# Kernel optimization log

Measured on AMD Instinct MI355X. Metric: run time of the kernel, lower is better.

Reference implementation:

```python
import jax, jax.numpy as jnp
import numpy as np

N_NODES = 100000
N_EDGES = 1600000
IN_DIM, HID_DIM, OUT_DIM = 128, 128, 64


def setup_inputs() -> dict:
    key = jax.random.key(0)
    ks = jax.random.split(key, 5)
    x = jax.random.normal(ks[0], (N_NODES, IN_DIM), dtype=jnp.float32)
    edge_index = jax.random.randint(ks[1], (2, N_EDGES), 0, N_NODES, dtype=jnp.int64)
    W1 = jax.random.normal(ks[2], (IN_DIM, HID_DIM), dtype=jnp.float32) * (1.0 / np.sqrt(IN_DIM))
    b1 = jnp.zeros((HID_DIM,), dtype=jnp.float32)
    W2 = jax.random.normal(ks[3], (HID_DIM, OUT_DIM), dtype=jnp.float32) * (1.0 / np.sqrt(HID_DIM))
    b2 = jnp.zeros((OUT_DIM,), dtype=jnp.float32)
    return {"x": x, "edge_index": edge_index, "W1": W1, "b1": b1, "W2": W2, "b2": b2}


def _gcn_conv(h, row, col, norm, b, n_nodes):
    # h: [N, F] already linearly transformed; message = norm_e * h[src]; scatter-add to dst
    msg = h[row] * norm[:, None]                      # [E+N, F]
    out = jax.ops.segment_sum(msg, col, num_segments=n_nodes)
    return out + b


def reference(x, edge_index, W1, b1, W2, b2):
    n = x.shape[0]
    loops = jnp.arange(n, dtype=edge_index.dtype)
    row = jnp.concatenate([edge_index[0], loops])     # sources (incl. self loops)
    col = jnp.concatenate([edge_index[1], loops])     # targets
    # symmetric normalization: deg over targets with unit edge weights
    deg = jax.ops.segment_sum(jnp.ones_like(col, dtype=x.dtype), col, num_segments=n)
    dinv = jnp.where(deg > 0, jax.lax.rsqrt(jnp.maximum(deg, 1.0)), 0.0)
    norm = dinv[row] * dinv[col]                      # [E+N]
    h = jax.nn.relu(_gcn_conv(x @ W1, row, col, norm, b1, n))
    out = _gcn_conv(h @ W2, row, col, norm, b2, n)
    return out.mean(axis=0)                           # [OUT_DIM]
```

## Files before the change

kernel.cpp:

```cpp
#include <hip/hip_runtime.h>

#define N_NODES 100000
#define N_EDGES 1600000
#define IN_DIM 128
#define HID_DIM 128
#define OUT_DIM 64
#define BKT_SHIFT 7
#define BKT_SIZE 128
#define NBKT ((N_NODES + BKT_SIZE - 1) / BKT_SIZE)
#define B1 256
#define HIST_N (NBKT * B1)
#define HIST_N2 (2 * HIST_N)
#define GEMM_BLKS ((N_NODES + 127) / 128)

typedef float v2f __attribute__((ext_vector_type(2)));
typedef float v4f __attribute__((ext_vector_type(4)));
typedef short v8s __attribute__((ext_vector_type(8)));

__device__ __forceinline__ unsigned int f2bf(float f) {
  unsigned int u = __float_as_uint(f);
  return (u + 0x7FFFu + ((u >> 16) & 1u)) >> 16;
}

template <bool HI>
__device__ __forceinline__ v2f cvt8(unsigned int u) {
  return __builtin_amdgcn_cvt_pk_f32_fp8((int)u, HI);
}

__device__ __forceinline__ float wdec(unsigned int p) {
  return __uint_as_float((p >> 17) << 16);
}

__device__ __forceinline__ void load4(const void* ei, int is64, int half, int base,
                                      int* v) {
  if (is64) {
    const long long* e = (const long long*)ei + (size_t)half * N_EDGES + base;
    longlong2 a = *(const longlong2*)e;
    longlong2 b = *(const longlong2*)(e + 2);
    v[0] = (int)a.x; v[1] = (int)a.y; v[2] = (int)b.x; v[3] = (int)b.y;
  } else {
    const int* e = (const int*)ei + (size_t)half * N_EDGES + base;
    int4 a = *(const int4*)e;
    v[0] = a.x; v[1] = a.y; v[2] = a.z; v[3] = a.w;
  }
}

__device__ __forceinline__ int detect64_block(const unsigned int* ei, int* sh) {
  if (threadIdx.x == 0) *sh = 0;
  __syncthreads();
  if (ei[1 + 2 * threadIdx.x] != 0u) *sh = 1;
  __syncthreads();
  return (*sh == 0) ? 1 : 0;
}

__global__ __launch_bounds__(256) void front_kernel(const float* __restrict__ x,
                                                    const float* __restrict__ W,
                                                    const void* ei,
                                                    unsigned int* __restrict__ G,
                                                    int* hist, float* S) {
  __shared__ __align__(16) char smem[2 * 128 * 136 * 2];
  if (blockIdx.x >= GEMM_BLKS) {
    int* hd = (int*)smem;
    int* hs = hd + NBKT;
    int* sh = hs + NBKT;
    const int hb = blockIdx.x - GEMM_BLKS;
    if (hb == 0 && threadIdx.x < HID_DIM) S[threadIdx.x] = 0.f;
    const int is64 = detect64_block((const unsigned int*)ei, sh);
    for (int k = threadIdx.x; k < NBKT; k += 256) { hd[k] = 0; hs[k] = 0; }
    __syncthreads();
    for (int g = hb * 256 + threadIdx.x; g < N_EDGES / 4; g += B1 * 256) {
      int r[4], c[4];
      load4(ei, is64, 0, g * 4, r);
      load4(ei, is64, 1, g * 4, c);
#pragma unroll
      for (int k = 0; k < 4; k++) {
        atomicAdd(&hd[c[k] >> BKT_SHIFT], 1);
        atomicAdd(&hs[r[k] >> BKT_SHIFT], 1);
      }
    }
    __syncthreads();
    for (int k = threadIdx.x; k < NBKT; k += 256) {
      hist[k * B1 + hb] = hd[k];
      hist[HIST_N + k * B1 + hb] = hs[k];
    }
    return;
  }
  typedef unsigned short us_row[136];
  us_row* lx = (us_row*)smem;
  us_row* lwt = (us_row*)(smem + 128 * 136 * 2);
  const int t = threadIdx.x;
  const int row0 = blockIdx.x * 128;

  {
    const float4* W4 = (const float4*)W;
    for (int it = 0; it < 16; ++it) {
      int idx = t + 256 * it;
      int k = idx >> 5, c4 = (idx & 31) * 4;
      float4 w = W4[idx];
      lwt[c4 + 0][k] = (unsigned short)f2bf(w.x);
      lwt[c4 + 1][k] = (unsigned short)f2bf(w.y);
      lwt[c4 + 2][k] = (unsigned short)f2bf(w.z);
      lwt[c4 + 3][k] = (unsigned short)f2bf(w.w);
    }
  }
  {
    const float4* x4 = (const float4*)(x + (size_t)row0 * IN_DIM);
    for (int it = 0; it < 16; ++it) {
      int idx = t + 256 * it;
      int r = idx >> 5, kq = (idx & 31) * 4;
      float4 v = make_float4(0.f, 0.f, 0.f, 0.f);
      if (row0 + r < N_NODES) v = x4[idx];
      unsigned int p0 = (f2bf(v.y) << 16) | f2bf(v.x);
      unsigned int p1 = (f2bf(v.w) << 16) | f2bf(v.z);
      *(uint2*)&lx[r][kq] = make_uint2(p0, p1);
    }
  }
  __syncthreads();

  const int lane = t & 63;
  const int wv = t >> 6;
  const int m0 = wv * 32;
  const int lrow = lane & 15;
  const int lk = (lane >> 4) * 8;

  v4f acc[2][8];
#pragma unroll
  for (int si = 0; si < 2; si++)
#pragma unroll
    for (int n = 0; n < 8; n++) acc[si][n] = (v4f){0.f, 0.f, 0.f, 0.f};

#pragma unroll
  for (int kk = 0; kk < 128; kk += 32) {
    v8s a0 = *(const v8s*)&lx[m0 + lrow][kk + lk];
    v8s a1 = *(const v8s*)&lx[m0 + 16 + lrow][kk + lk];
#pragma unroll
    for (int n = 0; n < 8; n++) {
      v8s b = *(const v8s*)&lwt[n * 16 + lrow][kk + lk];
      acc[0][n] = __builtin_amdgcn_mfma_f32_16x16x32_bf16(a0, b, acc[0][n], 0, 0, 0);
      acc[1][n] = __builtin_amdgcn_mfma_f32_16x16x32_bf16(a1, b, acc[1][n], 0, 0, 0);
    }
  }

  unsigned char* G8 = (unsigned char*)G;
#pragma unroll
  for (int si = 0; si < 2; si++)
#pragma unroll
    for (int n = 0; n < 8; n++) {
      int colg = n * 16 + (lane & 15);
#pragma unroll
      for (int i = 0; i < 4; i++) {
        int r = row0 + m0 + si * 16 + (lane >> 4) * 4 + i;
        if (r < N_NODES) {
          float v = acc[si][n][i];
          int pk = __builtin_amdgcn_cvt_pk_fp8_f32(v, v, 0, false);
          G8[(size_t)r * HID_DIM + colg] = (unsigned char)(pk & 0xFF);
        }
      }
    }
}

__global__ void scan1_kernel(int* arr, int* bsum, int n) {
  __shared__ int tmp[256];
  int i = blockIdx.x * 256 + threadIdx.x;
  int v = (i < n) ? arr[i] : 0;
  tmp[threadIdx.x] = v;
  __syncthreads();
  for (int off = 1; off < 256; off <<= 1) {
    int t2 = (threadIdx.x >= off) ? tmp[threadIdx.x - off] : 0;
    __syncthreads();
    tmp[threadIdx.x] += t2;
    __syncthreads();
  }
  if (i < n) arr[i] = tmp[threadIdx.x] - v;
  if (threadIdx.x == 255) bsum[blockIdx.x] = tmp[255];
}

__global__ void scan2_kernel(int* bsum, int nb) {
  __shared__ int tmp[1024];
  const int t = threadIdx.x;
  int v0 = (2 * t < nb) ? bsum[2 * t] : 0;
  int v1 = (2 * t + 1 < nb) ? bsum[2 * t + 1] : 0;
  int s = v0 + v1;
  tmp[t] = s;
  __syncthreads();
  for (int off = 1; off < 1024; off <<= 1) {
    int t2 = (t >= off) ? tmp[t - off] : 0;
    __syncthreads();
    tmp[t] += t2;
    __syncthreads();
  }
  int excl = tmp[t] - s;
  if (2 * t < nb) bsum[2 * t] = excl;
  if (2 * t + 1 < nb) bsum[2 * t + 1] = excl + v0;
}

__global__ __launch_bounds__(256) void scatter_kernel(const void* ei, const int* hist,
                                                      const int* bsum,
                                                      unsigned int* pairs) {
  __shared__ int cd[NBKT], cs[NBKT], sh[1];
  const int is64 = detect64_block((const unsigned int*)ei, sh);
  for (int k = threadIdx.x; k < NBKT; k += 256) {
    cd[k] = hist[k * B1 + blockIdx.x] + bsum[k];
    cs[k] = hist[HIST_N + k * B1 + blockIdx.x] + bsum[NBKT + k];
  }
  __syncthreads();
  for (int g = blockIdx.x * 256 + threadIdx.x; g < N_EDGES / 4; g += B1 * 256) {
    int r[4], c[4];
    load4(ei, is64, 0, g * 4, r);
    load4(ei, is64, 1, g * 4, c);
#pragma unroll
    for (int k = 0; k < 4; k++) {
      int pd = atomicAdd(&cd[c[k] >> BKT_SHIFT], 1);
      pairs[pd] = ((unsigned int)(c[k] & (BKT_SIZE - 1)) << 17) | (unsigned int)r[k];
      int ps = atomicAdd(&cs[r[k] >> BKT_SHIFT], 1);
      pairs[ps] = ((unsigned int)(r[k] & (BKT_SIZE - 1)) << 17) | (unsigned int)c[k];
    }
  }
}

__global__ __launch_bounds__(256) void csrA_kernel(const int* hist, const int* bsum,
                                                   const unsigned int* pairs,
                                                   int* rowptr, float* dinv) {
  __shared__ int cnt[BKT_SIZE], sc[BKT_SIZE];
  const int k = blockIdx.x;
  const int base = hist[k * B1] + bsum[k];
  const int end = (k == NBKT - 1) ? N_EDGES : hist[(k + 1) * B1] + bsum[k + 1];
  const int nseg = end - base;
  const int l = threadIdx.x;
  if (l < BKT_SIZE) cnt[l] = 0;
  __syncthreads();
  for (int i = l; i < nseg; i += 256) atomicAdd(&cnt[pairs[base + i] >> 17], 1);
  __syncthreads();
  if (l < BKT_SIZE) sc[l] = cnt[l];
  __syncthreads();
  for (int off = 1; off < BKT_SIZE; off <<= 1) {
    int v = (l < BKT_SIZE && l >= off) ? sc[l - off] : 0;
    __syncthreads();
    if (l < BKT_SIZE) sc[l] += v;
    __syncthreads();
  }
  if (l < BKT_SIZE) {
    int excl = sc[l] - cnt[l];
    int v = k * BKT_SIZE + l;
    if (v < N_NODES) {
      rowptr[v] = base + excl;
      dinv[v] = rsqrtf((float)(cnt[l] + 1));
    }
  }
  if (k == NBKT - 1 && l == 0) rowptr[N_NODES] = N_EDGES;
}

__global__ __launch_bounds__(256) void csrBout_kernel(const int* hist, const int* bsum,
                                                      const unsigned int* pairs,
                                                      const int* __restrict__ rowptr,
                                                      const float* __restrict__ dinv,
                                                      unsigned int* __restrict__ csr,
                                                      float* __restrict__ wacc) {
  if (blockIdx.x < NBKT) {
    __shared__ int cur[BKT_SIZE];
    const int k = blockIdx.x;
    const int base = hist[k * B1] + bsum[k];
    const int end = (k == NBKT - 1) ? N_EDGES : hist[(k + 1) * B1] + bsum[k + 1];
    const int nseg = end - base;
    const int l = threadIdx.x;
    if (l < BKT_SIZE) {
      int v = k * BKT_SIZE + l;
      cur[l] = (v < N_NODES) ? rowptr[v] : 0;
    }
    __syncthreads();
    for (int i = l; i < nseg; i += 256) {
      unsigned int pk = pairs[base + i];
      unsigned int src = pk & 0x1FFFFu;
      int pos = atomicAdd(&cur[pk >> 17], 1);
      unsigned int bits = f2bf(dinv[src]);
      csr[pos] = (bits << 17) | src;
    }
    return;
  }
  __shared__ float fb[BKT_SIZE];
  const int k = blockIdx.x - NBKT;
  const int base = hist[HIST_N + k * B1] + bsum[NBKT + k];
  const int end =
      (k == NBKT - 1) ? 2 * N_EDGES : hist[HIST_N + (k + 1) * B1] + bsum[NBKT + k + 1];
  if (threadIdx.x < BKT_SIZE) fb[threadIdx.x] = 0.f;
  __syncthreads();
  for (int i = base + threadIdx.x; i < end; i += 256) {
    unsigned int pk = pairs[i];
    atomicAdd(&fb[pk >> 17], dinv[pk & 0x1FFFFu]);
  }
  __syncthreads();
  int v = k * BKT_SIZE + threadIdx.x;
  if (threadIdx.x < BKT_SIZE && v < N_NODES) wacc[v] = fb[threadIdx.x];
}

__global__ __launch_bounds__(256) void aggregate_kernel(
    const unsigned int* __restrict__ G, const int* __restrict__ rowptr,
    const unsigned int* __restrict__ csr, const float* __restrict__ dinv,
    const float* __restrict__ wacc, const float* __restrict__ b1,
    float* __restrict__ S) {
  const int lane = threadIdx.x & 63;
  const int sub = lane & 31;
  const int half = lane >> 5;
  const int wid = blockIdx.x * 4 + (threadIdx.x >> 6);
  const int nwaves = gridDim.x * 4;
  const float4 b = ((const float4*)b1)[sub];
  v2f s01 = {0.f, 0.f}, s23 = {0.f, 0.f};

  for (int c = wid; c < N_NODES; c += nwaves) {
    const int start = rowptr[c];
    const int cnum = rowptr[c + 1] - start;
    const float d = dinv[c];
    v2f a01 = {0.f, 0.f}, a23 = {0.f, 0.f};
    if (half == 0) {
      unsigned int g = G[c * 32 + sub];
      a01 = cvt8<false>(g) * d;
      a23 = cvt8<true>(g) * d;
    }
    for (int j0 = 0; j0 < cnum; j0 += 64) {
      unsigned int pkl = 0;
      if (j0 + lane < cnum)
        pkl = __builtin_nontemporal_load(&csr[start + j0 + lane]);
      const int m = min(64, cnum - j0);
      int i = 0;
      for (; i + 8 <= m; i += 8) {
        unsigned int p0 = __shfl(pkl, i + half);
        unsigned int p1 = __shfl(pkl, i + 2 + half);
        unsigned int p2 = __shfl(pkl, i + 4 + half);
        unsigned int p3 = __shfl(pkl, i + 6 + half);
        unsigned int g0 = G[(p0 & 0x1FFFFu) * 32 + sub];
        unsigned int g1 = G[(p1 & 0x1FFFFu) * 32 + sub];
        unsigned int g2 = G[(p2 & 0x1FFFFu) * 32 + sub];
        unsigned int g3 = G[(p3 & 0x1FFFFu) * 32 + sub];
        float w0 = wdec(p0), w1 = wdec(p1), w2 = wdec(p2), w3 = wdec(p3);
        a01 += cvt8<false>(g0) * w0; a23 += cvt8<true>(g0) * w0;
        a01 += cvt8<false>(g1) * w1; a23 += cvt8<true>(g1) * w1;
        a01 += cvt8<false>(g2) * w2; a23 += cvt8<true>(g2) * w2;
        a01 += cvt8<false>(g3) * w3; a23 += cvt8<true>(g3) * w3;
      }
      for (; i + 2 <= m; i += 2) {
        unsigned int p = __shfl(pkl, i + half);
        unsigned int g = G[(p & 0x1FFFFu) * 32 + sub];
        float w = wdec(p);
        a01 += cvt8<false>(g) * w;
        a23 += cvt8<true>(g) * w;
      }
      if (i < m) {
        unsigned int p = __shfl(pkl, i);
        if (half == 0) {
          unsigned int g = G[(p & 0x1FFFFu) * 32 + sub];
          float w = wdec(p);
          a01 += cvt8<false>(g) * w;
          a23 += cvt8<true>(g) * w;
        }
      }
    }
    a01.x += __shfl(a01.x, sub + 32);
    a01.y += __shfl(a01.y, sub + 32);
    a23.x += __shfl(a23.x, sub + 32);
    a23.y += __shfl(a23.y, sub + 32);
    if (half == 0) {
      float wc = d * (wacc[c] + d);
      s01.x += wc * fmaxf(fmaf(d, a01.x, b.x), 0.f);
      s01.y += wc * fmaxf(fmaf(d, a01.y, b.y), 0.f);
      s23.x += wc * fmaxf(fmaf(d, a23.x, b.z), 0.f);
      s23.y += wc * fmaxf(fmaf(d, a23.y, b.w), 0.f);
    }
  }

  __shared__ float ls[HID_DIM];
  if (threadIdx.x < HID_DIM) ls[threadIdx.x] = 0.f;
  __syncthreads();
  if (half == 0) {
    atomicAdd(&ls[4 * sub + 0], s01.x);
    atomicAdd(&ls[4 * sub + 1], s01.y);
    atomicAdd(&ls[4 * sub + 2], s23.x);
    atomicAdd(&ls[4 * sub + 3], s23.y);
  }
  __syncthreads();
  if (threadIdx.x < HID_DIM) atomicAdd(&S[threadIdx.x], ls[threadIdx.x]);
}

__global__ void finish_kernel(const float* __restrict__ S, const float* __restrict__ W2,
                              const float* __restrict__ b2, float* __restrict__ out) {
  int j = threadIdx.x;
  float acc = 0.f;
  for (int k = 0; k < HID_DIM; k++) acc += S[k] * W2[k * OUT_DIM + j];
  out[j] = acc * (1.0f / N_NODES) + b2[j];
}

extern "C" void kernel_launch(void* const* d_in, const int* in_sizes, int n_in,
                              void* d_out, int out_size, void* d_ws, size_t ws_size,
                              hipStream_t stream) {
  const float* x  = (const float*)d_in[0];
  const void*  ei = d_in[1];
  const float* W1 = (const float*)d_in[2];
  const float* b1 = (const float*)d_in[3];
  const float* W2 = (const float*)d_in[4];
  const float* b2 = (const float*)d_in[5];
  float* out = (float*)d_out;

  char* p = (char*)d_ws;
  size_t off = 0;
  auto alloc = [&](size_t bytes) -> void* {
    void* r = p + off;
    off = (off + bytes + 63) & ~(size_t)63;
    return r;
  };
  int*   hist   = (int*)alloc((size_t)HIST_N2 * 4);
  int*   bsum   = (int*)alloc(2048 * 4);
  unsigned int* pairs = (unsigned int*)alloc((size_t)2 * N_EDGES * 4);
  int*   rowptr = (int*)alloc(((size_t)N_NODES + 1) * 4);
  unsigned int* csr = (unsigned int*)alloc((size_t)N_EDGES * 4);
  float* dinv   = (float*)alloc((size_t)N_NODES * 4);
  float* wacc   = (float*)alloc((size_t)N_NODES * 4);
  float* S      = (float*)alloc(HID_DIM * 4);
  unsigned int* G = (unsigned int*)alloc((size_t)N_NODES * HID_DIM);
  (void)ws_size; (void)n_in; (void)in_sizes; (void)out_size;

  const int NBH = HIST_N2 / 256;

  front_kernel<<<GEMM_BLKS + B1, 256, 0, stream>>>(x, W1, ei, G, hist, S);
  scan1_kernel<<<NBH, 256, 0, stream>>>(hist, bsum, HIST_N2);
  scan2_kernel<<<1, 1024, 0, stream>>>(bsum, NBH);
  scatter_kernel<<<B1, 256, 0, stream>>>(ei, hist, bsum, pairs);
  csrA_kernel<<<NBKT, 256, 0, stream>>>(hist, bsum, pairs, rowptr, dinv);
  csrBout_kernel<<<2 * NBKT, 256, 0, stream>>>(hist, bsum, pairs, rowptr, dinv, csr,
                                               wacc);
  aggregate_kernel<<<2048, 256, 0, stream>>>(G, rowptr, csr, dinv, wacc, b1, S);
  finish_kernel<<<1, 64, 0, stream>>>(S, W2, b2, out);
}
```

Baseline: 291.6 us.

## Split fp8 hidden features into two column planes and aggregate each separately

The GEMM output is stored as two planes of 64 fp8 columns each, and the aggregation kernel is launched once per plane. Each wave now handles four edges at a time with 16 lanes per edge instead of two edges with 32 lanes. The aim is for each plane's gather working set (about 6.4MB) to sit better in cache, and for each gather to touch a 64-byte row segment. The cost is reading the CSR indices and metadata twice, plus a second kernel launch.

```diff
diff --git a/kernel.cpp b/kernel.cpp
--- a/kernel.cpp
+++ b/kernel.cpp
@@ -56,7 +56,7 @@
 __global__ __launch_bounds__(256) void front_kernel(const float* __restrict__ x,
                                                     const float* __restrict__ W,
                                                     const void* ei,
-                                                    unsigned int* __restrict__ G,
+                                                    unsigned char* __restrict__ G8,
                                                     int* hist, float* S) {
   __shared__ __align__(16) char smem[2 * 128 * 136 * 2];
   if (blockIdx.x >= GEMM_BLKS) {
@@ -141,19 +141,19 @@
     }
   }
 
-  unsigned char* G8 = (unsigned char*)G;
 #pragma unroll
   for (int si = 0; si < 2; si++)
 #pragma unroll
     for (int n = 0; n < 8; n++) {
       int colg = n * 16 + (lane & 15);
+      size_t pbase = (size_t)(colg >> 6) * N_NODES * 64 + (colg & 63);
 #pragma unroll
       for (int i = 0; i < 4; i++) {
         int r = row0 + m0 + si * 16 + (lane >> 4) * 4 + i;
         if (r < N_NODES) {
           float v = acc[si][n][i];
           int pk = __builtin_amdgcn_cvt_pk_fp8_f32(v, v, 0, false);
-          G8[(size_t)r * HID_DIM + colg] = (unsigned char)(pk & 0xFF);
+          G8[pbase + (size_t)r * 64] = (unsigned char)(pk & 0xFF);
         }
       }
     }
@@ -294,16 +294,16 @@
 }
 
 __global__ __launch_bounds__(256) void aggregate_kernel(
-    const unsigned int* __restrict__ G, const int* __restrict__ rowptr,
+    const unsigned int* __restrict__ Gp, const int* __restrict__ rowptr,
     const unsigned int* __restrict__ csr, const float* __restrict__ dinv,
-    const float* __restrict__ wacc, const float* __restrict__ b1,
-    float* __restrict__ S) {
+    const float* __restrict__ wacc, const float* __restrict__ b1p,
+    float* __restrict__ Sp) {
   const int lane = threadIdx.x & 63;
-  const int sub = lane & 31;
-  const int half = lane >> 5;
+  const int q = lane & 15;
+  const int slot = lane >> 4;
   const int wid = blockIdx.x * 4 + (threadIdx.x >> 6);
   const int nwaves = gridDim.x * 4;
-  const float4 b = ((const float4*)b1)[sub];
+  const float4 b = ((const float4*)b1p)[q];
   v2f s01 = {0.f, 0.f}, s23 = {0.f, 0.f};
 
   for (int c = wid; c < N_NODES; c += nwaves) {
@@ -311,8 +311,8 @@
     const int cnum = rowptr[c + 1] - start;
     const float d = dinv[c];
     v2f a01 = {0.f, 0.f}, a23 = {0.f, 0.f};
-    if (half == 0) {
-      unsigned int g = G[c * 32 + sub];
+    if (slot == 0) {
+      unsigned int g = Gp[c * 16 + q];
       a01 = cvt8<false>(g) * d;
       a23 = cvt8<true>(g) * d;
     }
@@ -322,43 +322,38 @@
         pkl = __builtin_nontemporal_load(&csr[start + j0 + lane]);
       const int m = min(64, cnum - j0);
       int i = 0;
-      for (; i + 8 <= m; i += 8) {
-        unsigned int p0 = __shfl(pkl, i + half);
-        unsigned int p1 = __shfl(pkl, i + 2 + half);
-        unsigned int p2 = __shfl(pkl, i + 4 + half);
-        unsigned int p3 = __shfl(pkl, i + 6 + half);
-        unsigned int g0 = G[(p0 & 0x1FFFFu) * 32 + sub];
-        unsigned int g1 = G[(p1 & 0x1FFFFu) * 32 + sub];
-        unsigned int g2 = G[(p2 & 0x1FFFFu) * 32 + sub];
-        unsigned int g3 = G[(p3 & 0x1FFFFu) * 32 + sub];
+      for (; i + 16 <= m; i += 16) {
+        unsigned int p0 = __shfl(pkl, i + slot);
+        unsigned int p1 = __shfl(pkl, i + 4 + slot);
+        unsigned int p2 = __shfl(pkl, i + 8 + slot);
+        unsigned int p3 = __shfl(pkl, i + 12 + slot);
+        unsigned int g0 = Gp[(p0 & 0x1FFFFu) * 16 + q];
+        unsigned int g1 = Gp[(p1 & 0x1FFFFu) * 16 + q];
+        unsigned int g2 = Gp[(p2 & 0x1FFFFu) * 16 + q];
+        unsigned int g3 = Gp[(p3 & 0x1FFFFu) * 16 + q];
         float w0 = wdec(p0), w1 = wdec(p1), w2 = wdec(p2), w3 = wdec(p3);
         a01 += cvt8<false>(g0) * w0; a23 += cvt8<true>(g0) * w0;
         a01 += cvt8<false>(g1) * w1; a23 += cvt8<true>(g1) * w1;
         a01 += cvt8<false>(g2) * w2; a23 += cvt8<true>(g2) * w2;
         a01 += cvt8<false>(g3) * w3; a23 += cvt8<true>(g3) * w3;
       }
-      for (; i + 2 <= m; i += 2) {
-        unsigned int p = __shfl(pkl, i + half);
-        unsigned int g = G[(p & 0x1FFFFu) * 32 + sub];
-        float w = wdec(p);
+      for (; i < m; i += 4) {
+        int e = i + slot;
+        unsigned int pv = __shfl(pkl, min(e, m - 1));
+        float w = (e < m) ? wdec(pv) : 0.f;
+        unsigned int g = Gp[(pv & 0x1FFFFu) * 16 + q];
         a01 += cvt8<false>(g) * w;
         a23 += cvt8<true>(g) * w;
       }
-      if (i < m) {
-        unsigned int p = __shfl(pkl, i);
-        if (half == 0) {
-          unsigned int g = G[(p & 0x1FFFFu) * 32 + sub];
-          float w = wdec(p);
-          a01 += cvt8<false>(g) * w;
-          a23 += cvt8<true>(g) * w;
-        }
-      }
-    }
-    a01.x += __shfl(a01.x, sub + 32);
-    a01.y += __shfl(a01.y, sub + 32);
-    a23.x += __shfl(a23.x, sub + 32);
-    a23.y += __shfl(a23.y, sub + 32);
-    if (half == 0) {
+    }
+#pragma unroll
+    for (int off = 16; off < 64; off <<= 1) {
+      a01.x += __shfl_xor(a01.x, off);
+      a01.y += __shfl_xor(a01.y, off);
+      a23.x += __shfl_xor(a23.x, off);
+      a23.y += __shfl_xor(a23.y, off);
+    }
+    if (slot == 0) {
       float wc = d * (wacc[c] + d);
       s01.x += wc * fmaxf(fmaf(d, a01.x, b.x), 0.f);
       s01.y += wc * fmaxf(fmaf(d, a01.y, b.y), 0.f);
@@ -367,17 +362,17 @@
     }
   }
 
-  __shared__ float ls[HID_DIM];
-  if (threadIdx.x < HID_DIM) ls[threadIdx.x] = 0.f;
-  __syncthreads();
-  if (half == 0) {
-    atomicAdd(&ls[4 * sub + 0], s01.x);
-    atomicAdd(&ls[4 * sub + 1], s01.y);
-    atomicAdd(&ls[4 * sub + 2], s23.x);
-    atomicAdd(&ls[4 * sub + 3], s23.y);
-  }
-  __syncthreads();
-  if (threadIdx.x < HID_DIM) atomicAdd(&S[threadIdx.x], ls[threadIdx.x]);
+  __shared__ float ls[64];
+  if (threadIdx.x < 64) ls[threadIdx.x] = 0.f;
+  __syncthreads();
+  if (slot == 0) {
+    atomicAdd(&ls[4 * q + 0], s01.x);
+    atomicAdd(&ls[4 * q + 1], s01.y);
+    atomicAdd(&ls[4 * q + 2], s23.x);
+    atomicAdd(&ls[4 * q + 3], s23.y);
+  }
+  __syncthreads();
+  if (threadIdx.x < 64) atomicAdd(&Sp[threadIdx.x], ls[threadIdx.x]);
 }
 
 __global__ void finish_kernel(const float* __restrict__ S, const float* __restrict__ W2,
@@ -418,8 +413,10 @@
   (void)ws_size; (void)n_in; (void)in_sizes; (void)out_size;
 
   const int NBH = HIST_N2 / 256;
-
-  front_kernel<<<GEMM_BLKS + B1, 256, 0, stream>>>(x, W1, ei, G, hist, S);
+  const size_t PLANE = (size_t)N_NODES * 16;
+
+  front_kernel<<<GEMM_BLKS + B1, 256, 0, stream>>>(x, W1, ei, (unsigned char*)G, hist,
+                                                   S);
   scan1_kernel<<<NBH, 256, 0, stream>>>(hist, bsum, HIST_N2);
   scan2_kernel<<<1, 1024, 0, stream>>>(bsum, NBH);
   scatter_kernel<<<B1, 256, 0, stream>>>(ei, hist, bsum, pairs);
@@ -427,5 +424,7 @@
   csrBout_kernel<<<2 * NBKT, 256, 0, stream>>>(hist, bsum, pairs, rowptr, dinv, csr,
                                                wacc);
   aggregate_kernel<<<2048, 256, 0, stream>>>(G, rowptr, csr, dinv, wacc, b1, S);
+  aggregate_kernel<<<2048, 256, 0, stream>>>(G + PLANE, rowptr, csr, dinv, wacc,
+                                             b1 + 64, S + 64);
   finish_kernel<<<1, 64, 0, stream>>>(S, W2, b2, out);
 }
```

New measurement: 329.9 us. 1.13x slower.
